# Kernel tuning notes

Hardware: AMD Instinct MI355X
Metric: run time of the kernel (lower is better)

Reference implementation:

```python
import jax, jax.numpy as jnp
import numpy as np

N, K, IN_C, OUT_C = 100000, 128, 128, 128


def setup_inputs() -> dict:
    key = jax.random.key(0)
    k1, k2, k3 = jax.random.split(key, 3)
    x = jax.random.normal(k1, (N, IN_C), dtype=jnp.float32)
    U = jax.random.normal(k2, (N, K), dtype=jnp.float32)
    coeffs = jax.random.normal(k3, (OUT_C, K, IN_C), dtype=jnp.float32)
    return {"x": x, "U": U, "coeffs": coeffs}


def reference(x, U, coeffs):
    # U.T @ x : (K, in_channels)
    spec = jnp.einsum('nk,ni->ki', U, x)
    # coeffs * spec, summed over in_channels : (out_channels, K)
    mixed = jnp.einsum('oki,ki->ok', coeffs, spec)
    # U @ mixed : (out_channels, N)
    out = jnp.einsum('nk,ok->on', U, mixed)
    # softmax over N (dim=-1), then transpose -> (N, out_channels)
    return jax.nn.softmax(out, axis=-1).T
```

## Files before the change

### kernel.cpp

```cpp
#include <hip/hip_runtime.h>
#include <math.h>

#define N_PTS 100000
#define KDIM 128
#define CDIM 128
#define TILE_N 64
#define NB1 ((N_PTS + TILE_N - 1) / TILE_N)

typedef short s16x8 __attribute__((ext_vector_type(8)));
typedef float f32x4 __attribute__((ext_vector_type(4)));

static __device__ __forceinline__ unsigned short f2bf(float f) {
    unsigned int u = __float_as_uint(f);
    unsigned int r = (u + 0x7FFFu + ((u >> 16) & 1u)) >> 16;
    return (unsigned short)r;
}
static __device__ __forceinline__ float bf2f(unsigned short h) {
    return __uint_as_float(((unsigned int)h) << 16);
}

static __device__ __forceinline__ void split_trunc(float v, unsigned short& hi, unsigned short& lo) {
    unsigned int u = __float_as_uint(v);
    unsigned int uh = u & 0xFFFF0000u;
    float lf = v - __uint_as_float(uh);
    hi = (unsigned short)(u >> 16);
    lo = (unsigned short)(__float_as_uint(lf) >> 16);
}

__global__ __launch_bounds__(512) void kA(const float* __restrict__ U,
                                          const float* __restrict__ x,
                                          float* __restrict__ partials,
                                          int chunk) {
    const int tid = threadIdx.x;
    const int b = blockIdx.x;
    const int n_begin = b * chunk;
    const int n_end = min(N_PTS, n_begin + chunk);
    const int lane = tid & 63;
    const int w = tid >> 6;
    const int mtb = (w & 3) * 2;
    const int ntb = (w >> 2) * 4;
    const int quad = lane >> 4;
    const int nl = lane & 15;

    f32x4 acc[2][4];
#pragma unroll
    for (int mi = 0; mi < 2; ++mi)
#pragma unroll
        for (int ni = 0; ni < 4; ++ni) acc[mi][ni] = (f32x4)(0.0f);

    for (int r0 = n_begin; r0 < n_end; r0 += 32) {
        const int rb = r0 + 8 * quad;
        s16x8 ah[2], al[2];
        {
            const float* ubase = U + (size_t)rb * 128 + mtb * 16 + nl;
#pragma unroll
            for (int mi = 0; mi < 2; ++mi) {
                float v[8];
#pragma unroll
                for (int j = 0; j < 8; ++j) v[j] = ubase[(size_t)j * 128 + mi * 16];
                s16x8 hh, ll;
#pragma unroll
                for (int j = 0; j < 8; ++j) {
                    unsigned short h, l;
                    split_trunc(v[j], h, l);
                    hh[j] = (short)h; ll[j] = (short)l;
                }
                ah[mi] = hh; al[mi] = ll;
            }
        }
        {
            const float* xbase = x + (size_t)rb * 128 + ntb * 16 + nl;
#pragma unroll
            for (int ni = 0; ni < 4; ++ni) {
                float v[8];
#pragma unroll
                for (int j = 0; j < 8; ++j) v[j] = xbase[(size_t)j * 128 + ni * 16];
                s16x8 bh, bl;
#pragma unroll
                for (int j = 0; j < 8; ++j) {
                    unsigned short h, l;
                    split_trunc(v[j], h, l);
                    bh[j] = (short)h; bl[j] = (short)l;
                }
#pragma unroll
                for (int mi = 0; mi < 2; ++mi) {
                    acc[mi][ni] = __builtin_amdgcn_mfma_f32_16x16x32_bf16(ah[mi], bh, acc[mi][ni], 0, 0, 0);
                    acc[mi][ni] = __builtin_amdgcn_mfma_f32_16x16x32_bf16(al[mi], bh, acc[mi][ni], 0, 0, 0);
                    acc[mi][ni] = __builtin_amdgcn_mfma_f32_16x16x32_bf16(ah[mi], bl, acc[mi][ni], 0, 0, 0);
                }
            }
        }
    }

    float* p = partials + (size_t)b * 16384;
#pragma unroll
    for (int mi = 0; mi < 2; ++mi) {
#pragma unroll
        for (int reg = 0; reg < 4; ++reg) {
            int k = (mtb + mi) * 16 + quad * 4 + reg;
#pragma unroll
            for (int ni = 0; ni < 4; ++ni) {
                int i = (ntb + ni) * 16 + nl;
                p[k * 128 + i] = acc[mi][ni][reg];
            }
        }
    }
}

__global__ __launch_bounds__(256) void kA2a(const float* __restrict__ partials,
                                            float* __restrict__ partial2, int nA) {
    const int jc = blockIdx.x >> 3;
    const int s = blockIdx.x & 7;
    const int j = jc * 256 + threadIdx.x;
    const int per = (nA + 7) >> 3;
    int b = s * per;
    const int be = min(b + per, nA);
    float a0 = 0.0f, a1 = 0.0f, a2 = 0.0f, a3 = 0.0f;
    for (; b + 4 <= be; b += 4) {
        a0 += partials[(size_t)(b + 0) * 16384 + j];
        a1 += partials[(size_t)(b + 1) * 16384 + j];
        a2 += partials[(size_t)(b + 2) * 16384 + j];
        a3 += partials[(size_t)(b + 3) * 16384 + j];
    }
    for (; b < be; ++b) a0 += partials[(size_t)b * 16384 + j];
    partial2[(size_t)s * 16384 + j] = (a0 + a1) + (a2 + a3);
}

__global__ __launch_bounds__(256) void kB(const float* __restrict__ coeffs,
                                          const float* __restrict__ partial2,
                                          unsigned short* __restrict__ afrag_hi,
                                          unsigned short* __restrict__ afrag_lo) {
    int wave = (blockIdx.x * 256 + threadIdx.x) >> 6;
    int lane = threadIdx.x & 63;
    int o = wave >> 7;
    int k = wave & 127;
    const int j = k * 128 + lane * 2;
    float2 p0 = *(const float2*)&partial2[j];
    float2 p1 = *(const float2*)&partial2[16384 + j];
    float2 p2 = *(const float2*)&partial2[2 * 16384 + j];
    float2 p3 = *(const float2*)&partial2[3 * 16384 + j];
    float2 p4 = *(const float2*)&partial2[4 * 16384 + j];
    float2 p5 = *(const float2*)&partial2[5 * 16384 + j];
    float2 p6 = *(const float2*)&partial2[6 * 16384 + j];
    float2 p7 = *(const float2*)&partial2[7 * 16384 + j];
    float sx = ((p0.x + p1.x) + (p2.x + p3.x)) + ((p4.x + p5.x) + (p6.x + p7.x));
    float sy = ((p0.y + p1.y) + (p2.y + p3.y)) + ((p4.y + p5.y) + (p6.y + p7.y));
    float2 c2 = *(const float2*)&coeffs[((size_t)o * 128 + k) * 128 + lane * 2];
    float v = c2.x * sx + c2.y * sy;
#pragma unroll
    for (int s = 32; s >= 1; s >>= 1) v += __shfl_xor(v, s);
    if (lane == 0) {
        unsigned short hi = f2bf(v);
        unsigned short lo = f2bf(v - bf2f(hi));
        int idx = ((o >> 4) * 4 + (k >> 5)) * 512 + (((k >> 3) & 3) * 16 + (o & 15)) * 8 + (k & 7);
        afrag_hi[idx] = hi;
        afrag_lo[idx] = lo;
    }
}

__global__ __launch_bounds__(512) void kC1(const float* __restrict__ U,
                                           const unsigned short* __restrict__ afrag_hi,
                                           const unsigned short* __restrict__ afrag_lo,
                                           float* __restrict__ out,
                                           float* __restrict__ m_part,
                                           float* __restrict__ l_part) {
    __shared__ unsigned short Bh[8192];
    __shared__ unsigned short Bl[8192];
    const int tid = threadIdx.x;
    const int b = blockIdx.x;
    const int n0 = b * TILE_N;
    const int lane = tid & 63;
    const int w = tid >> 6;
    const int quad = lane >> 4;
    const int nl = lane & 15;

    {
        const int sn = tid & 63;
        const int k8b = tid >> 6;
        const int gn = n0 + sn;
#pragma unroll
        for (int r = 0; r < 2; ++r) {
            const int k0 = (k8b + r * 8) * 8;
            float4 f0 = make_float4(0, 0, 0, 0), f1 = make_float4(0, 0, 0, 0);
            if (gn < N_PTS) {
                f0 = *(const float4*)&U[(size_t)gn * 128 + k0];
                f1 = *(const float4*)&U[(size_t)gn * 128 + k0 + 4];
            }
            float vv[8] = {f0.x, f0.y, f0.z, f0.w, f1.x, f1.y, f1.z, f1.w};
            s16x8 hh, ll;
#pragma unroll
            for (int jj = 0; jj < 8; ++jj) {
                unsigned short h, l;
                split_trunc(vv[jj], h, l);
                hh[jj] = (short)h;
                ll[jj] = (short)l;
            }
            const int T = (k0 >> 5) * 4 + (sn >> 4);
            const int g = T * 64 + ((k0 >> 3) & 3) * 16 + ((sn & 15) ^ (T & 3));
            *(s16x8*)&Bh[g * 8] = hh;
            *(s16x8*)&Bl[g * 8] = ll;
        }
    }

    s16x8 Ah[4], Al[4];
#pragma unroll
    for (int kc = 0; kc < 4; ++kc) {
        size_t aoff = (size_t)(w * 4 + kc) * 512 + lane * 8;
        Ah[kc] = *(const s16x8*)(afrag_hi + aoff);
        Al[kc] = *(const s16x8*)(afrag_lo + aoff);
    }

    __syncthreads();

    f32x4 acc[4];
#pragma unroll
    for (int nt = 0; nt < 4; ++nt) acc[nt] = (f32x4)(0.0f);

#pragma unroll
    for (int kc = 0; kc < 4; ++kc) {
#pragma unroll
        for (int nt = 0; nt < 4; ++nt) {
            const int T = kc * 4 + nt;
            const int g = T * 64 + quad * 16 + (nl ^ (T & 3));
            s16x8 bh = *(s16x8*)&Bh[g * 8];
            s16x8 bl = *(s16x8*)&Bl[g * 8];
            acc[nt] = __builtin_amdgcn_mfma_f32_16x16x32_bf16(Ah[kc], bh, acc[nt], 0, 0, 0);
            acc[nt] = __builtin_amdgcn_mfma_f32_16x16x32_bf16(Al[kc], bh, acc[nt], 0, 0, 0);
            acc[nt] = __builtin_amdgcn_mfma_f32_16x16x32_bf16(Ah[kc], bl, acc[nt], 0, 0, 0);
        }
    }

#pragma unroll
    for (int nt = 0; nt < 4; ++nt) {
        if (n0 + nt * 16 + nl >= N_PTS) {
#pragma unroll
            for (int reg = 0; reg < 4; ++reg) acc[nt][reg] = -3.4e38f;
        }
    }

    float mb[4];
#pragma unroll
    for (int reg = 0; reg < 4; ++reg)
        mb[reg] = fmaxf(fmaxf(acc[0][reg], acc[1][reg]), fmaxf(acc[2][reg], acc[3][reg]));
#pragma unroll
    for (int s = 1; s < 16; s <<= 1) {
#pragma unroll
        for (int reg = 0; reg < 4; ++reg) mb[reg] = fmaxf(mb[reg], __shfl_xor(mb[reg], s));
    }

#pragma unroll
    for (int nt = 0; nt < 4; ++nt) {
#pragma unroll
        for (int reg = 0; reg < 4; ++reg) acc[nt][reg] = __expf(acc[nt][reg] - mb[reg]);
        int gn = n0 + nt * 16 + nl;
        if (gn < N_PTS)
            *(f32x4*)&out[(size_t)gn * 128 + w * 16 + quad * 4] = acc[nt];
    }

    float ls[4];
#pragma unroll
    for (int reg = 0; reg < 4; ++reg)
        ls[reg] = ((acc[0][reg] + acc[1][reg]) + (acc[2][reg] + acc[3][reg]));
#pragma unroll
    for (int s = 1; s < 16; s <<= 1) {
#pragma unroll
        for (int reg = 0; reg < 4; ++reg) ls[reg] += __shfl_xor(ls[reg], s);
    }

    if (nl == 0) {
#pragma unroll
        for (int reg = 0; reg < 4; ++reg) {
            int o = w * 16 + quad * 4 + reg;
            m_part[(size_t)o * NB1 + b] = mb[reg];
            l_part[(size_t)o * NB1 + b] = ls[reg];
        }
    }
}

__global__ __launch_bounds__(256) void kC2(const float* __restrict__ m_part,
                                           const float* __restrict__ l_part,
                                           float* __restrict__ scale) {
    const int o = blockIdx.x;
    const int tid = threadIdx.x;
    const float* __restrict__ mp = m_part + (size_t)o * NB1;
    const float* __restrict__ lp = l_part + (size_t)o * NB1;
    __shared__ float sm[256];
    float m = -3.4e38f;
    for (int b = tid; b < NB1; b += 256) m = fmaxf(m, mp[b]);
    sm[tid] = m;
    __syncthreads();
    for (int s = 128; s >= 1; s >>= 1) {
        if (tid < s) sm[tid] = fmaxf(sm[tid], sm[tid + s]);
        __syncthreads();
    }
    m = sm[0];
    __syncthreads();
    float l = 0.0f;
    for (int b = tid; b < NB1; b += 256)
        l += lp[b] * __expf(mp[b] - m);
    sm[tid] = l;
    __syncthreads();
    for (int s = 128; s >= 1; s >>= 1) {
        if (tid < s) sm[tid] += sm[tid + s];
        __syncthreads();
    }
    l = sm[0];
    float inv = 1.0f / l;
    for (int b = tid; b < NB1; b += 256)
        scale[(size_t)o * NB1 + b] = __expf(mp[b] - m) * inv;
}

__global__ __launch_bounds__(256) void kC3(float* __restrict__ out,
                                           const float* __restrict__ scale) {
    const int b = blockIdx.x;
    const int tid = threadIdx.x;
    __shared__ float sc[128];
    if (tid < 128) sc[tid] = scale[(size_t)tid * NB1 + b];
    __syncthreads();
    const int n0 = b * TILE_N;
#pragma unroll
    for (int r = 0; r < 8; ++r) {
        int idx = (r * 256 + tid) * 4;
        int n = idx >> 7;
        int o = idx & 127;
        int gn = n0 + n;
        if (gn < N_PTS) {
            float4 v = *(float4*)&out[(size_t)gn * 128 + o];
            v.x *= sc[o];
            v.y *= sc[o + 1];
            v.z *= sc[o + 2];
            v.w *= sc[o + 3];
            *(float4*)&out[(size_t)gn * 128 + o] = v;
        }
    }
}

extern "C" void kernel_launch(void* const* d_in, const int* in_sizes, int n_in,
                              void* d_out, int out_size, void* d_ws, size_t ws_size,
                              hipStream_t stream) {
    const float* x = (const float*)d_in[0];
    const float* U = (const float*)d_in[1];
    const float* coeffs = (const float*)d_in[2];
    float* out = (float*)d_out;

    float* f = (float*)d_ws;
    float* spec = f;
    unsigned short* afrag_hi = (unsigned short*)(f + 16384);
    unsigned short* afrag_lo = (unsigned short*)(f + 16384 + 8192);
    float* m_part = f + 16384 + 16384;
    float* l_part = m_part + (size_t)128 * NB1;
    float* scale = l_part + (size_t)128 * NB1;
    float* partial2 = scale + (size_t)128 * NB1;
    float* partialsA = partial2 + 8 * 16384;
    (void)spec;

    size_t fixed_bytes = ((size_t)(16384 * 2) + (size_t)NB1 * 128 * 3 + (size_t)8 * 16384) * 4;
    int nA = 512;
    if (ws_size > fixed_bytes) {
        size_t avail = (ws_size - fixed_bytes) / 65536;
        if ((size_t)nA > avail) nA = (int)avail;
    } else {
        nA = 1;
    }
    if (nA < 1) nA = 1;
    int chunk = (((N_PTS + nA - 1) / nA) + 31) & ~31;
    int nB = (N_PTS + chunk - 1) / chunk;

    kA<<<nB, 512, 0, stream>>>(U, x, partialsA, chunk);
    kA2a<<<512, 256, 0, stream>>>(partialsA, partial2, nB);
    kB<<<4096, 256, 0, stream>>>(coeffs, partial2, afrag_hi, afrag_lo);
    kC1<<<NB1, 512, 0, stream>>>(U, afrag_hi, afrag_lo, out, m_part, l_part);
    kC2<<<128, 256, 0, stream>>>(m_part, l_part, scale);
    kC3<<<NB1, 256, 0, stream>>>(out, scale);
}
```

Before: 214.2 us.

## Fuse projection, softmax stats and normalization into one cooperative kernel

```diff
diff --git a/kernel.cpp b/kernel.cpp
--- a/kernel.cpp
+++ b/kernel.cpp
@@ -1,11 +1,16 @@
 #include <hip/hip_runtime.h>
+#include <hip/hip_cooperative_groups.h>
 #include <math.h>
+
+namespace cg = cooperative_groups;
 
 #define N_PTS 100000
 #define KDIM 128
 #define CDIM 128
 #define TILE_N 64
 #define NB1 ((N_PTS + TILE_N - 1) / TILE_N)
+#define CT 4
+#define CGRID ((NB1 + CT - 1) / CT)
 
 typedef short s16x8 __attribute__((ext_vector_type(8)));
 typedef float f32x4 __attribute__((ext_vector_type(4)));
@@ -111,19 +116,17 @@
                                             float* __restrict__ partial2, int nA) {
     const int jc = blockIdx.x >> 3;
     const int s = blockIdx.x & 7;
-    const int j = jc * 256 + threadIdx.x;
+    const int j = jc * 1024 + threadIdx.x * 4;
     const int per = (nA + 7) >> 3;
     int b = s * per;
     const int be = min(b + per, nA);
-    float a0 = 0.0f, a1 = 0.0f, a2 = 0.0f, a3 = 0.0f;
-    for (; b + 4 <= be; b += 4) {
-        a0 += partials[(size_t)(b + 0) * 16384 + j];
-        a1 += partials[(size_t)(b + 1) * 16384 + j];
-        a2 += partials[(size_t)(b + 2) * 16384 + j];
-        a3 += partials[(size_t)(b + 3) * 16384 + j];
-    }
-    for (; b < be; ++b) a0 += partials[(size_t)b * 16384 + j];
-    partial2[(size_t)s * 16384 + j] = (a0 + a1) + (a2 + a3);
+    f32x4 a0 = (f32x4)(0.0f), a1 = (f32x4)(0.0f);
+    for (; b + 2 <= be; b += 2) {
+        a0 += *(const f32x4*)&partials[(size_t)(b + 0) * 16384 + j];
+        a1 += *(const f32x4*)&partials[(size_t)(b + 1) * 16384 + j];
+    }
+    for (; b < be; ++b) a0 += *(const f32x4*)&partials[(size_t)b * 16384 + j];
+    *(f32x4*)&partial2[(size_t)s * 16384 + j] = a0 + a1;
 }
 
 __global__ __launch_bounds__(256) void kB(const float* __restrict__ coeffs,
@@ -158,6 +161,188 @@
     }
 }
 
+__global__ __launch_bounds__(512, 4) void kCC(const float* __restrict__ U,
+                                              const unsigned short* __restrict__ afrag_hi,
+                                              const unsigned short* __restrict__ afrag_lo,
+                                              float* __restrict__ m_part,
+                                              float* __restrict__ l_part,
+                                              float* __restrict__ ML,
+                                              float* __restrict__ out) {
+    cg::grid_group gg = cg::this_grid();
+    __shared__ unsigned short Bh[8192];
+    __shared__ unsigned short Bl[8192];
+    __shared__ float sm[512];
+    const int tid = threadIdx.x;
+    const int lane = tid & 63;
+    const int w = tid >> 6;
+    const int quad = lane >> 4;
+    const int nl = lane & 15;
+
+    f32x4 acc[CT][4];
+    float mbv[CT][4];
+
+#pragma unroll
+    for (int t = 0; t < CT; ++t) {
+        const int b = blockIdx.x * CT + t;
+        if (b < NB1) {
+            const int n0 = b * TILE_N;
+            {
+                const int sn = tid & 63;
+                const int k8b = tid >> 6;
+                const int gn = n0 + sn;
+#pragma unroll
+                for (int r = 0; r < 2; ++r) {
+                    const int k0 = (k8b + r * 8) * 8;
+                    float4 f0 = make_float4(0, 0, 0, 0), f1 = make_float4(0, 0, 0, 0);
+                    if (gn < N_PTS) {
+                        f0 = *(const float4*)&U[(size_t)gn * 128 + k0];
+                        f1 = *(const float4*)&U[(size_t)gn * 128 + k0 + 4];
+                    }
+                    float vv[8] = {f0.x, f0.y, f0.z, f0.w, f1.x, f1.y, f1.z, f1.w};
+                    s16x8 hh, ll;
+#pragma unroll
+                    for (int jj = 0; jj < 8; ++jj) {
+                        unsigned short h, l;
+                        split_trunc(vv[jj], h, l);
+                        hh[jj] = (short)h;
+                        ll[jj] = (short)l;
+                    }
+                    const int T = (k0 >> 5) * 4 + (sn >> 4);
+                    const int g = T * 64 + ((k0 >> 3) & 3) * 16 + ((sn & 15) ^ (T & 3));
+                    *(s16x8*)&Bh[g * 8] = hh;
+                    *(s16x8*)&Bl[g * 8] = ll;
+                }
+            }
+            __syncthreads();
+
+#pragma unroll
+            for (int nt = 0; nt < 4; ++nt) acc[t][nt] = (f32x4)(0.0f);
+
+#pragma unroll
+            for (int kc = 0; kc < 4; ++kc) {
+                size_t aoff = (size_t)(w * 4 + kc) * 512 + lane * 8;
+                s16x8 Ah = *(const s16x8*)(afrag_hi + aoff);
+                s16x8 Al = *(const s16x8*)(afrag_lo + aoff);
+#pragma unroll
+                for (int nt = 0; nt < 4; ++nt) {
+                    const int T = kc * 4 + nt;
+                    const int g = T * 64 + quad * 16 + (nl ^ (T & 3));
+                    s16x8 bh = *(s16x8*)&Bh[g * 8];
+                    s16x8 bl = *(s16x8*)&Bl[g * 8];
+                    acc[t][nt] = __builtin_amdgcn_mfma_f32_16x16x32_bf16(Ah, bh, acc[t][nt], 0, 0, 0);
+                    acc[t][nt] = __builtin_amdgcn_mfma_f32_16x16x32_bf16(Al, bh, acc[t][nt], 0, 0, 0);
+                    acc[t][nt] = __builtin_amdgcn_mfma_f32_16x16x32_bf16(Ah, bl, acc[t][nt], 0, 0, 0);
+                }
+            }
+            __syncthreads();
+
+#pragma unroll
+            for (int nt = 0; nt < 4; ++nt) {
+                if (n0 + nt * 16 + nl >= N_PTS) {
+#pragma unroll
+                    for (int reg = 0; reg < 4; ++reg) acc[t][nt][reg] = -3.4e38f;
+                }
+            }
+            float mb[4];
+#pragma unroll
+            for (int reg = 0; reg < 4; ++reg)
+                mb[reg] = fmaxf(fmaxf(acc[t][0][reg], acc[t][1][reg]),
+                                fmaxf(acc[t][2][reg], acc[t][3][reg]));
+#pragma unroll
+            for (int s = 1; s < 16; s <<= 1) {
+#pragma unroll
+                for (int reg = 0; reg < 4; ++reg) mb[reg] = fmaxf(mb[reg], __shfl_xor(mb[reg], s));
+            }
+#pragma unroll
+            for (int reg = 0; reg < 4; ++reg) mbv[t][reg] = mb[reg];
+
+            float ls[4];
+#pragma unroll
+            for (int reg = 0; reg < 4; ++reg) {
+                float e0 = __expf(acc[t][0][reg] - mb[reg]);
+                float e1 = __expf(acc[t][1][reg] - mb[reg]);
+                float e2 = __expf(acc[t][2][reg] - mb[reg]);
+                float e3 = __expf(acc[t][3][reg] - mb[reg]);
+                ls[reg] = (e0 + e1) + (e2 + e3);
+            }
+#pragma unroll
+            for (int s = 1; s < 16; s <<= 1) {
+#pragma unroll
+                for (int reg = 0; reg < 4; ++reg) ls[reg] += __shfl_xor(ls[reg], s);
+            }
+            if (nl == 0) {
+#pragma unroll
+                for (int reg = 0; reg < 4; ++reg) {
+                    int o = w * 16 + quad * 4 + reg;
+                    m_part[(size_t)o * NB1 + b] = mb[reg];
+                    l_part[(size_t)o * NB1 + b] = ls[reg];
+                }
+            }
+        } else {
+#pragma unroll
+            for (int nt = 0; nt < 4; ++nt) acc[t][nt] = (f32x4)(0.0f);
+#pragma unroll
+            for (int reg = 0; reg < 4; ++reg) mbv[t][reg] = 0.0f;
+        }
+    }
+
+    gg.sync();
+
+    if (blockIdx.x < 128) {
+        const int o = blockIdx.x;
+        const float* __restrict__ mp = m_part + (size_t)o * NB1;
+        const float* __restrict__ lp = l_part + (size_t)o * NB1;
+        float m = -3.4e38f;
+        for (int b2 = tid; b2 < NB1; b2 += 512) m = fmaxf(m, mp[b2]);
+        sm[tid] = m;
+        __syncthreads();
+        for (int s = 256; s >= 1; s >>= 1) {
+            if (tid < s) sm[tid] = fmaxf(sm[tid], sm[tid + s]);
+            __syncthreads();
+        }
+        m = sm[0];
+        __syncthreads();
+        float l = 0.0f;
+        for (int b2 = tid; b2 < NB1; b2 += 512) l += lp[b2] * __expf(mp[b2] - m);
+        sm[tid] = l;
+        __syncthreads();
+        for (int s = 256; s >= 1; s >>= 1) {
+            if (tid < s) sm[tid] += sm[tid + s];
+            __syncthreads();
+        }
+        if (tid == 0) {
+            ML[o] = m;
+            ML[128 + o] = 1.0f / sm[0];
+        }
+    }
+
+    gg.sync();
+
+#pragma unroll
+    for (int t = 0; t < CT; ++t) {
+        const int b = blockIdx.x * CT + t;
+        if (b < NB1) {
+            const int n0 = b * TILE_N;
+            float fac[4];
+#pragma unroll
+            for (int reg = 0; reg < 4; ++reg) {
+                int o = w * 16 + quad * 4 + reg;
+                fac[reg] = __expf(mbv[t][reg] - ML[o]) * ML[128 + o];
+            }
+#pragma unroll
+            for (int nt = 0; nt < 4; ++nt) {
+                f32x4 v;
+#pragma unroll
+                for (int reg = 0; reg < 4; ++reg)
+                    v[reg] = __expf(acc[t][nt][reg] - mbv[t][reg]) * fac[reg];
+                int gn = n0 + nt * 16 + nl;
+                if (gn < N_PTS)
+                    *(f32x4*)&out[(size_t)gn * 128 + w * 16 + quad * 4] = v;
+            }
+        }
+    }
+}
+
 __global__ __launch_bounds__(512) void kC1(const float* __restrict__ U,
                                            const unsigned short* __restrict__ afrag_hi,
                                            const unsigned short* __restrict__ afrag_lo,
@@ -367,9 +552,22 @@
     int nB = (N_PTS + chunk - 1) / chunk;
 
     kA<<<nB, 512, 0, stream>>>(U, x, partialsA, chunk);
-    kA2a<<<512, 256, 0, stream>>>(partialsA, partial2, nB);
+    kA2a<<<128, 256, 0, stream>>>(partialsA, partial2, nB);
     kB<<<4096, 256, 0, stream>>>(coeffs, partial2, afrag_hi, afrag_lo);
-    kC1<<<NB1, 512, 0, stream>>>(U, afrag_hi, afrag_lo, out, m_part, l_part);
-    kC2<<<128, 256, 0, stream>>>(m_part, l_part, scale);
-    kC3<<<NB1, 256, 0, stream>>>(out, scale);
-}
+
+    bool coop_ok = false;
+    int maxb = 0;
+    if (hipOccupancyMaxActiveBlocksPerMultiprocessor(&maxb, (const void*)kCC, 512, 0) == hipSuccess &&
+        (long)maxb * 256 >= CGRID) {
+        void* args[] = {(void*)&U, (void*)&afrag_hi, (void*)&afrag_lo,
+                        (void*)&m_part, (void*)&l_part, (void*)&scale, (void*)&out};
+        if (hipLaunchCooperativeKernel((const void*)kCC, dim3(CGRID), dim3(512),
+                                       args, 0, stream) == hipSuccess)
+            coop_ok = true;
+    }
+    if (!coop_ok) {
+        kC1<<<NB1, 512, 0, stream>>>(U, afrag_hi, afrag_lo, out, m_part, l_part);
+        kC2<<<128, 256, 0, stream>>>(m_part, l_part, scale);
+        kC3<<<NB1, 256, 0, stream>>>(out, scale);
+    }
+}
```

After: 219.0 us. +2.2%, slower.
